# Kernel tuning notes

Hardware: AMD Instinct MI355X
Metric: run time of the kernel (lower is better)

Reference implementation:

```python
import jax, jax.numpy as jnp
import numpy as np

ATOM_TYPES = [1, 6, 7, 8, 16]
GRID_LENGTHS = [8.0, 12.0]
GRID_SIZE = 16


def _make_grid(L, G):
    # vertices of the cubic grid, (G, G, G, 3), matching torch generate_grid (ij ordering)
    ticks = jnp.linspace(-L / 2.0, L / 2.0, G)
    return jnp.stack(jnp.meshgrid(ticks, ticks, ticks, indexing='ij'), axis=-1)


def reference(distance_vector, sigma, atomic_numbers):
    # distance_vector: (B, A, N, 3); atomic_numbers: (A, N); sigma: (1,)
    coeff = -0.5 / (sigma ** 2)  # (1,)
    reps = []
    for Z in ATOM_TYPES:
        mask = (atomic_numbers == Z).astype(distance_vector.dtype)  # (A, N)
        d = distance_vector * mask[None, :, :, None]                # (B, A, N, 3)
        d_sq = jnp.sum(d * d, axis=-1)                              # (B, A, N)
        for L in GRID_LENGTHS:
            grid = _make_grid(L, GRID_SIZE)                         # (G, G, G, 3)
            g_sq = jnp.sum(grid * grid, axis=-1)                    # (G, G, G)
            # ||grid - d||^2 = |grid|^2 + |d|^2 - 2 d.grid  (avoids (...,3) broadcast)
            dot = jnp.einsum('banc,xyzc->banxyz', d, grid)          # (B, A, N, G, G, G)
            sq = g_sq[None, None, None] + d_sq[..., None, None, None] - 2.0 * dot
            box = jnp.exp(coeff * sq).sum(axis=2)                   # (B, A, G, G, G)
            reps.append(box)
    return jnp.stack(reps, axis=2)  # (B, A, C, G, G, G)


def setup_inputs() -> dict:
    key = jax.random.key(0)
    k1, k2 = jax.random.split(key)
    distance_vector = jax.random.normal(k1, (1, 128, 64, 3), dtype=jnp.float32) * 3.0
    atomic_numbers = jax.random.randint(k2, (128, 64), 0, 17).astype(jnp.int64)
    sigma = jnp.ones((1,), dtype=jnp.float32)
    return {'distance_vector': distance_vector, 'sigma': sigma, 'atomic_numbers': atomic_numbers}
```

## Files before the change

kernel.cpp:

```cpp
#include <hip/hip_runtime.h>

static constexpr int kA = 128;
static constexpr int kN = 64;
static constexpr int kG = 16;
static constexpr int kC = 10;


__global__ __launch_bounds__(256) void voxel_kernel(
    const float* __restrict__ dvec,
    const float* __restrict__ sigma,
    const int*   __restrict__ zn,
    float*       __restrict__ out)
{
    const int blk = blockIdx.x;
    const int a   = blk / 10;
    const int c   = blk - a * 10;
    const int ch  = c >> 1;
    const int li  = c & 1;

    const int Ztab[5] = {1, 6, 7, 8, 16};
    const int Ztarget = Ztab[ch];

    const float Lg   = li ? 12.0f : 8.0f;
    const float step = Lg * (1.0f / 15.0f);
    const float t0   = -0.5f * Lg;
    const float sg   = sigma[0];
    const float coeff = -0.5f / (sg * sg);

    const int t = threadIdx.x;

    __shared__ float s_tab[3 * kN * kG];
    __shared__ float s_e0[kG];

    if (t < 192) {
        const float d  = dvec[(size_t)a * (kN * 3) + t];
        const int   n  = t / 3;
        const int   ax = t - 3 * n;
        float* dst = &s_tab[(ax * kN + n) * kG];
#pragma unroll
        for (int i = 0; i < kG; ++i) {
            const float r = (t0 + i * step) - d;
            dst[i] = __expf(coeff * r * r);
        }
    } else if (t < 192 + kG) {
        const int i = t - 192;
        const float r = t0 + i * step;
        s_e0[i] = __expf(coeff * r * r);
    }

    const int lane = t & 63;
    const int Zl   = zn[a * kN + lane];
    unsigned long long mask = __ballot(Zl == Ztarget);
    const int cnt = __popcll(mask);

    __syncthreads();

    const int y  = (t >> 2) & 15;
    const int zq = (t & 3) * 4;
    const int xb = t >> 6;

    const float* s_ex = &s_tab[0 * kN * kG];
    const float* s_ey = &s_tab[1 * kN * kG];
    const float* s_ez = &s_tab[2 * kN * kG];

    float acc[4][4];
    {
        const float w  = (float)(kN - cnt) * s_e0[y];
        float ez0[4];
#pragma unroll
        for (int j = 0; j < 4; ++j) ez0[j] = s_e0[zq + j];
#pragma unroll
        for (int i = 0; i < 4; ++i) {
            const float wx = w * s_e0[xb + 4 * i];
#pragma unroll
            for (int j = 0; j < 4; ++j)
                acc[i][j] = wx * ez0[j];
        }
    }

    while (mask) {
        const int n = (int)__builtin_ctzll(mask);
        mask &= mask - 1ull;
        const float eyn = s_ey[n * kG + y];
        float ezn[4];
#pragma unroll
        for (int j = 0; j < 4; ++j) ezn[j] = s_ez[n * kG + zq + j];
#pragma unroll
        for (int i = 0; i < 4; ++i) {
            const float p = s_ex[n * kG + xb + 4 * i] * eyn;
#pragma unroll
            for (int j = 0; j < 4; ++j)
                acc[i][j] = fmaf(p, ezn[j], acc[i][j]);
        }
    }

    float4* o = (float4*)(out + ((size_t)a * kC + c) * (kG * kG * kG));
#pragma unroll
    for (int q = 0; q < 4; ++q)
        o[t + 256 * q] = make_float4(acc[q][0], acc[q][1], acc[q][2], acc[q][3]);
}

extern "C" void kernel_launch(void* const* d_in, const int* in_sizes, int n_in,
                              void* d_out, int out_size, void* d_ws, size_t ws_size,
                              hipStream_t stream) {
    const float* dvec  = (const float*)d_in[0];
    const float* sigma = (const float*)d_in[1];
    const int*   zn    = (const int*)d_in[2];
    float* out = (float*)d_out;

    voxel_kernel<<<dim3(kA * kC), dim3(256), 0, stream>>>(dvec, sigma, zn, out);
}
```

Before: 65.52 us.

## Replace shared-memory exp tables with per-thread exp and wave shuffles

The block no longer precomputes per-atom, per-axis Gaussian factor tables in LDS and no longer waits on a __syncthreads barrier. Each lane loads one atom's coordinates, and inside the atom loop the coordinates are broadcast with __shfl. Each thread then computes its own 9 exponentials per matching atom. This removes the LDS setup, the barrier and the shared-memory reads, at the cost of redundant transcendental work in the inner loop.

```diff
diff --git a/kernel.cpp b/kernel.cpp
--- a/kernel.cpp
+++ b/kernel.cpp
@@ -27,51 +27,40 @@
     const float sg   = sigma[0];
     const float coeff = -0.5f / (sg * sg);
 
-    const int t = threadIdx.x;
+    const int t    = threadIdx.x;
+    const int lane = t & 63;
 
-    __shared__ float s_tab[3 * kN * kG];
-    __shared__ float s_e0[kG];
+    const int   Zl  = zn[a * kN + lane];
+    const float* dl = dvec + ((size_t)a * kN + lane) * 3;
+    const float dxl = dl[0];
+    const float dyl = dl[1];
+    const float dzl = dl[2];
 
-    if (t < 192) {
-        const float d  = dvec[(size_t)a * (kN * 3) + t];
-        const int   n  = t / 3;
-        const int   ax = t - 3 * n;
-        float* dst = &s_tab[(ax * kN + n) * kG];
-#pragma unroll
-        for (int i = 0; i < kG; ++i) {
-            const float r = (t0 + i * step) - d;
-            dst[i] = __expf(coeff * r * r);
-        }
-    } else if (t < 192 + kG) {
-        const int i = t - 192;
-        const float r = t0 + i * step;
-        s_e0[i] = __expf(coeff * r * r);
-    }
-
-    const int lane = t & 63;
-    const int Zl   = zn[a * kN + lane];
     unsigned long long mask = __ballot(Zl == Ztarget);
     const int cnt = __popcll(mask);
-
-    __syncthreads();
 
     const int y  = (t >> 2) & 15;
     const int zq = (t & 3) * 4;
     const int xb = t >> 6;
-
-    const float* s_ex = &s_tab[0 * kN * kG];
-    const float* s_ey = &s_tab[1 * kN * kG];
-    const float* s_ez = &s_tab[2 * kN * kG];
+    const float gy = t0 + y * step;
+    float gxv[4], gzv[4];
+#pragma unroll
+    for (int i = 0; i < 4; ++i) gxv[i] = t0 + (xb + 4 * i) * step;
+#pragma unroll
+    for (int j = 0; j < 4; ++j) gzv[j] = t0 + (zq + j) * step;
 
     float acc[4][4];
     {
-        const float w  = (float)(kN - cnt) * s_e0[y];
-        float ez0[4];
+        const float w  = (float)(kN - cnt);
+        const float ey0 = __expf(coeff * gy * gy);
+        float ex0[4], ez0[4];
 #pragma unroll
-        for (int j = 0; j < 4; ++j) ez0[j] = s_e0[zq + j];
+        for (int i = 0; i < 4; ++i) ex0[i] = __expf(coeff * gxv[i] * gxv[i]);
+#pragma unroll
+        for (int j = 0; j < 4; ++j) ez0[j] = __expf(coeff * gzv[j] * gzv[j]);
 #pragma unroll
         for (int i = 0; i < 4; ++i) {
-            const float wx = w * s_e0[xb + 4 * i];
+            const float wx = w * ey0 * ex0[i];
 #pragma unroll
             for (int j = 0; j < 4; ++j)
                 acc[i][j] = wx * ez0[j];
@@ -81,16 +70,29 @@
     while (mask) {
         const int n = (int)__builtin_ctzll(mask);
         mask &= mask - 1ull;
-        const float eyn = s_ey[n * kG + y];
-        float ezn[4];
-#pragma unroll
-        for (int j = 0; j < 4; ++j) ezn[j] = s_ez[n * kG + zq + j];
+        const float dx = __shfl(dxl, n);
+        const float dy = __shfl(dyl, n);
+        const float dz = __shfl(dzl, n);
+
+        const float ry = gy - dy;
+        const float py = __expf(coeff * ry * ry);
+        float ex[4], ez[4];
 #pragma unroll
         for (int i = 0; i < 4; ++i) {
-            const float p = s_ex[n * kG + xb + 4 * i] * eyn;
+            const float rx = gxv[i] - dx;
+            ex[i] = __expf(coeff * rx * rx);
+        }
+#pragma unroll
+        for (int j = 0; j < 4; ++j) {
+            const float rz = gzv[j] - dz;
+            ez[j] = __expf(coeff * rz * rz);
+        }
+#pragma unroll
+        for (int i = 0; i < 4; ++i) {
+            const float pxy = ex[i] * py;
 #pragma unroll
             for (int j = 0; j < 4; ++j)
-                acc[i][j] = fmaf(p, ezn[j], acc[i][j]);
+                acc[i][j] = fmaf(pxy, ez[j], acc[i][j]);
         }
     }
 
```

New measurement: 66.48 us. Within noise of the previous version (+1.5%).
